# Performance work log

Hardware: AMD Instinct MI355X
Metric: run time of the kernel (lower is better)

The kernel has to match this reference:

```python
import jax, jax.numpy as jnp
import numpy as np

N_NODES = 100000
N_EDGES = 3200000


def setup_inputs() -> dict:
    key = jax.random.key(0)
    ks = jax.random.split(key, 12)
    x = jax.random.normal(ks[0], (N_NODES, 5), dtype=jnp.float32)
    edges = jax.random.randint(ks[1], (2, N_EDGES), 0, N_NODES)
    edge_attr = jax.random.normal(ks[2], (N_EDGES, 2), dtype=jnp.float32)
    detector_labels = jax.random.bernoulli(ks[3], 0.7, (N_NODES,))

    def init(k, shape, fan_in):
        return (jax.random.normal(k, shape, dtype=jnp.float32) / np.sqrt(fan_in)).astype(jnp.float32)

    W_gat = init(ks[4], (5, 16), 5)        # GATConv lin (shared src/dst)
    att_src = init(ks[5], (16,), 16)
    att_dst = init(ks[6], (16,), 16)
    W_edge = init(ks[7], (2, 16), 2)       # GATConv lin_edge
    att_edge = init(ks[8], (16,), 16)
    b_gat = jnp.zeros((16,), jnp.float32)
    W1 = init(ks[9], (34, 64), 34)
    b1 = jnp.zeros((64,), jnp.float32)
    W2 = init(ks[10], (64, 2), 64)
    b2 = jnp.zeros((2,), jnp.float32)
    return dict(x=x, edges=edges, edge_attr=edge_attr, detector_labels=detector_labels,
                W_gat=W_gat, att_src=att_src, att_dst=att_dst, W_edge=W_edge,
                att_edge=att_edge, b_gat=b_gat, W1=W1, b1=b1, W2=W2, b2=b2)


def reference(x, edges, edge_attr, detector_labels, W_gat, att_src, att_dst,
              W_edge, att_edge, b_gat, W1, b1, W2, b2):
    n_nodes = x.shape[0]
    src, dst = edges[0], edges[1]

    # --- GATConv(5 -> 16, heads=1, concat=False, edge_dim=2, no self loops) ---
    h = x @ W_gat                                        # [N, 16]
    a_src = h @ att_src                                  # [N]
    a_dst = h @ att_dst                                  # [N]
    a_edge = (edge_attr @ W_edge) @ att_edge             # [E]
    alpha = jax.nn.leaky_relu(a_src[src] + a_dst[dst] + a_edge, 0.2)
    # segmented softmax over incoming edges of each dst node
    seg_max = jax.ops.segment_max(alpha, dst, num_segments=n_nodes)
    ex = jnp.exp(alpha - seg_max[dst])
    denom = jax.ops.segment_sum(ex, dst, num_segments=n_nodes)
    a = ex / (denom[dst] + 1e-16)                        # [E]
    out = jax.ops.segment_sum(h[src] * a[:, None], dst, num_segments=n_nodes) + b_gat
    xh = jax.nn.relu(out)                                # [N, 16]

    # --- edge update: gather-concat-MLP ---
    feat = jnp.concatenate([xh[src], edge_attr, xh[dst]], axis=-1)   # [E, 34]
    ef = jax.nn.relu(feat @ W1 + b1) @ W2 + b2                       # [E, 2]

    # --- SplitSyndromes: keep edges whose both endpoints are detectors ---
    valid = detector_labels[src] & detector_labels[dst]
    idx = jnp.nonzero(valid)[0]        # eager (data-dependent size, not jitted)
    return edges[:, idx], jax.nn.sigmoid(ef[idx])
```

## Files before the change

kernel.cpp:

```cpp
#include <hip/hip_runtime.h>

#define NN 100000
#define NE 3200000
#define CH 8192
#define NCB ((NE + CH - 1) / CH)
#define ITER (CH / 256)
#define NBK ((NN + 63) >> 6)
#define CAP 2560

typedef __attribute__((ext_vector_type(8))) __bf16 bf16x8;
typedef __attribute__((ext_vector_type(4))) float f32x4;

union BF8 { unsigned short u[8]; bf16x8 v; };

__global__ void kdetect(const unsigned char* __restrict__ lab8, int* __restrict__ flags) {
  __shared__ int tmp[256];
  int t = threadIdx.x;
  int s = 0;
  for (int i = t; i < 25000; i += 256) s += lab8[4 * i + 1];
  tmp[t] = s;
  __syncthreads();
  for (int d = 128; d > 0; d >>= 1) { if (t < d) tmp[t] += tmp[t + d]; __syncthreads(); }
  if (t == 0) flags[0] = (tmp[0] != 0) ? 1 : 0;
}

__global__ void klab(const void* __restrict__ lab, const int* __restrict__ flags,
                     int* __restrict__ labN) {
  int n = blockIdx.x * 256 + threadIdx.x;
  if (n >= NN) return;
  int v;
  if (flags[0]) v = ((const unsigned char*)lab)[n];
  else          v = ((const int*)lab)[n];
  labN[n] = (v != 0) ? 1 : 0;
}

__global__ void kc01(const float* __restrict__ We, const float* __restrict__ ae,
                     float* __restrict__ c01) {
  if (threadIdx.x == 0) {
    float c0 = 0.f, c1 = 0.f;
    for (int k = 0; k < 16; k++) { c0 += We[k] * ae[k]; c1 += We[16 + k] * ae[k]; }
    c01[0] = c0; c01[1] = c1;
  }
}

__global__ void knodeA(const float* __restrict__ x, const float* __restrict__ Wg,
                       const float* __restrict__ atts, const float* __restrict__ attd,
                       float* __restrict__ a_src, float* __restrict__ a_dst) {
  int n = blockIdx.x * 256 + threadIdx.x;
  if (n >= NN) return;
  float xi[5];
#pragma unroll
  for (int i = 0; i < 5; i++) xi[i] = x[n * 5 + i];
  float asum = 0.f, dsum = 0.f;
#pragma unroll
  for (int k = 0; k < 16; k++) {
    float acc = 0.f;
#pragma unroll
    for (int i = 0; i < 5; i++) acc += xi[i] * Wg[i * 16 + k];
    asum += acc * atts[k];
    dsum += acc * attd[k];
  }
  a_src[n] = asum; a_dst[n] = dsum;
}

__global__ __launch_bounds__(256) void khist(const int* __restrict__ src,
                                             const int* __restrict__ dst,
                                             const int* __restrict__ labN,
                                             int* __restrict__ blkcnt,
                                             int* __restrict__ cntc) {
  __shared__ int hist[NBK];
  __shared__ int vsum;
  int tid = threadIdx.x, b = blockIdx.x;
  for (int i = tid; i < NBK; i += 256) hist[i] = 0;
  if (tid == 0) vsum = 0;
  __syncthreads();
  int wsum = 0;
  for (int it = 0; it < ITER; ++it) {
    int e = b * CH + it * 256 + tid;
    int v = 0;
    if (e < NE) {
      int s = src[e], d = dst[e];
      atomicAdd(&hist[d >> 6], 1);
      v = labN[s] & labN[d];
    }
    unsigned long long m = __ballot(v != 0);
    wsum += __popcll(m);
  }
  if ((tid & 63) == 0) atomicAdd(&vsum, wsum);
  __syncthreads();
  for (int i = tid; i < NBK; i += 256) blkcnt[i * NCB + b] = hist[i];
  if (tid == 0) cntc[b] = vsum;
}

__global__ __launch_bounds__(256) void kscanb(int* __restrict__ blkcnt,
                                              int* __restrict__ total) {
  __shared__ int a[512];
  int row = blockIdx.x, t = threadIdx.x;
  int* p = blkcnt + row * NCB;
  int o0 = (t < NCB) ? p[t] : 0;
  int o1 = (t + 256 < NCB) ? p[t + 256] : 0;
  a[t] = o0; a[t + 256] = o1;
  __syncthreads();
  for (int d = 1; d < 512; d <<= 1) {
    int x0 = (t >= d) ? a[t - d] : 0;
    int x1 = (t + 256 >= d) ? a[t + 256 - d] : 0;
    __syncthreads();
    a[t] += x0; a[t + 256] += x1;
    __syncthreads();
  }
  if (t < NCB) p[t] = a[t] - o0;
  if (t + 256 < NCB) p[t + 256] = a[t + 256] - o1;
  if (t == 0) total[row] = a[NCB - 1];
}

__global__ void kscan(const int* __restrict__ cnt, int* __restrict__ off, int nb) {
  __shared__ int tmp[256];
  __shared__ int carry;
  int t = threadIdx.x;
  if (t == 0) carry = 0;
  __syncthreads();
  for (int base = 0; base < nb; base += 256) {
    int i = base + t;
    int v = (i < nb) ? cnt[i] : 0;
    tmp[t] = v;
    __syncthreads();
    for (int d = 1; d < 256; d <<= 1) {
      int add = (t >= d) ? tmp[t - d] : 0;
      __syncthreads();
      tmp[t] += add;
      __syncthreads();
    }
    if (i < nb) off[i] = carry + tmp[t] - v;
    __syncthreads();
    if (t == 0) carry += tmp[255];
    __syncthreads();
  }
  if (t == 0) off[nb] = carry;
}

__global__ __launch_bounds__(256) void kscat(
    const int* __restrict__ src, const int* __restrict__ dst,
    const float* __restrict__ eattr, const int* __restrict__ labN,
    const float* __restrict__ a_src, const float* __restrict__ a_dst,
    const float* __restrict__ c01, const int* __restrict__ bucket_base,
    const int* __restrict__ blkcnt, const int* __restrict__ offc,
    uint2* __restrict__ bins, float* __restrict__ out,
    float2* __restrict__ eat2, int NV) {
  __shared__ int cur[NBK];
  __shared__ int wc[4];
  __shared__ int lbase;
  int b = blockIdx.x, tid = threadIdx.x;
  for (int i = tid; i < NBK; i += 256) cur[i] = bucket_base[i] + blkcnt[i * NCB + b];
  if (tid == 0) lbase = offc[b];
  float c0 = c01[0], c1 = c01[1];
  __syncthreads();
  int lane = tid & 63, wid = tid >> 6;
  for (int it = 0; it < ITER; ++it) {
    int e = b * CH + it * 256 + tid;
    int v = 0, s = 0, d = 0;
    float2 ea;
    if (e < NE) {
      s = src[e]; d = dst[e];
      ea = ((const float2*)eattr)[e];
      float al = a_src[s] + a_dst[d] + ea.x * c0 + ea.y * c1;
      al = (al > 0.f) ? al : 0.2f * al;
      float exv = __expf(al);
      int pos = atomicAdd(&cur[d >> 6], 1);
      uint2 pl;
      pl.x = ((unsigned)s << 6) | (unsigned)(d & 63);
      pl.y = __float_as_uint(exv);
      bins[pos] = pl;
      v = labN[s] & labN[d];
    }
    unsigned long long m = __ballot(v != 0);
    if (lane == 0) wc[wid] = __popcll(m);
    __syncthreads();
    int pre = 0;
    for (int i = 0; i < wid; i++) pre += wc[i];
    pre += __popcll(m & ((1ull << lane) - 1ull));
    if (v) {
      int p = lbase + pre;
      if (p < NV) {
        out[p] = (float)s;
        out[NV + p] = (float)d;
        eat2[p] = ea;
      }
    }
    __syncthreads();
    if (tid == 0) lbase += wc[0] + wc[1] + wc[2] + wc[3];
  }
}

__global__ __launch_bounds__(512) void kagg(
    const uint2* __restrict__ bins, const int* __restrict__ bucket_base,
    const float* __restrict__ x, const float* __restrict__ Wg,
    const float* __restrict__ bg, float* __restrict__ xh) {
  __shared__ uint2 pay[CAP];
  __shared__ int cnt[64], inc[64], cur[64];
  __shared__ float sWg[80], sbg[16];
  int k = blockIdx.x, tid = threadIdx.x;
  if (tid < 80) sWg[tid] = Wg[tid];
  else if (tid < 96) sbg[tid - 80] = bg[tid - 80];
  int start = bucket_base[k], end = bucket_base[k + 1];
  int node0 = k << 6;
  int c = tid & 15, g = tid >> 4;
  __syncthreads();
  float w0 = sWg[c], w1 = sWg[16 + c], w2 = sWg[32 + c], w3 = sWg[48 + c], w4 = sWg[64 + c];
  float acc[2] = {0.f, 0.f}, den[2] = {0.f, 0.f};
  for (int cb = start; cb < end; cb += CAP) {
    int n = min(end - cb, CAP);
    if (tid < 64) cnt[tid] = 0;
    __syncthreads();
    uint2 st0, st1, st2, st3, st4;
    {
      int i;
      i = tid;          if (i < n) { st0 = bins[cb + i]; atomicAdd(&cnt[st0.x & 63], 1); }
      i = tid + 512;    if (i < n) { st1 = bins[cb + i]; atomicAdd(&cnt[st1.x & 63], 1); }
      i = tid + 1024;   if (i < n) { st2 = bins[cb + i]; atomicAdd(&cnt[st2.x & 63], 1); }
      i = tid + 1536;   if (i < n) { st3 = bins[cb + i]; atomicAdd(&cnt[st3.x & 63], 1); }
      i = tid + 2048;   if (i < n) { st4 = bins[cb + i]; atomicAdd(&cnt[st4.x & 63], 1); }
    }
    __syncthreads();
    if (tid < 64) inc[tid] = cnt[tid];
    __syncthreads();
    for (int d = 1; d < 64; d <<= 1) {
      int v = 0;
      if (tid >= d && tid < 64) v = inc[tid - d];
      __syncthreads();
      if (tid < 64) inc[tid] += v;
      __syncthreads();
    }
    if (tid < 64) cur[tid] = inc[tid] - cnt[tid];
    __syncthreads();
    {
      int i;
      i = tid;          if (i < n) pay[atomicAdd(&cur[st0.x & 63], 1)] = st0;
      i = tid + 512;    if (i < n) pay[atomicAdd(&cur[st1.x & 63], 1)] = st1;
      i = tid + 1024;   if (i < n) pay[atomicAdd(&cur[st2.x & 63], 1)] = st2;
      i = tid + 1536;   if (i < n) pay[atomicAdd(&cur[st3.x & 63], 1)] = st3;
      i = tid + 2048;   if (i < n) pay[atomicAdd(&cur[st4.x & 63], 1)] = st4;
    }
    __syncthreads();
#pragma unroll
    for (int p = 0; p < 2; ++p) {
      int nd = p * 32 + g;
      int re = inc[nd], rs = re - cnt[nd];
      float a = 0.f, ds = 0.f;
      for (int idx = rs; idx < re; ++idx) {
        uint2 pl = pay[idx];
        int s = (int)(pl.x >> 6);
        float exv = __uint_as_float(pl.y);
        const float* xp = x + s * 5;
        float h = xp[0] * w0 + xp[1] * w1 + xp[2] * w2 + xp[3] * w3 + xp[4] * w4;
        a += h * exv;
        ds += exv;
      }
      acc[p] += a; den[p] += ds;
    }
    __syncthreads();
  }
#pragma unroll
  for (int p = 0; p < 2; ++p) {
    int node = node0 + p * 32 + g;
    if (node < NN) {
      float dn = fmaxf(den[p], 1e-30f);
      float v = acc[p] / dn + sbg[c];
      xh[node * 16 + c] = (v > 0.f) ? v : 0.f;
    }
  }
}

__global__ __launch_bounds__(256) void kmlp(
    const float2* __restrict__ eat2, const float* __restrict__ xh,
    const float* __restrict__ W1, const float* __restrict__ b1,
    const float* __restrict__ W2, const float* __restrict__ b2,
    float* __restrict__ out, int NV) {
  int tid = threadIdx.x;
  int lane = tid & 63, wid = tid >> 6;
  int lo4 = lane & 15, q = lane >> 4;

  BF8 bh[4], bl[4];
#pragma unroll
  for (int ct = 0; ct < 4; ct++) {
    int col = ct * 16 + lo4;
#pragma unroll
    for (int i = 0; i < 8; i++) {
      int k = q * 8 + i;
      int r = (k < 16) ? k : (k + 2);
      float w = W1[r * 64 + col];
      unsigned u = __float_as_uint(w);
      float rem = w - __uint_as_float(u & 0xffff0000u);
      bh[ct].u[i] = (unsigned short)(u >> 16);
      bl[ct].u[i] = (unsigned short)(__float_as_uint(rem) >> 16);
    }
  }
  float b1v[4], w16v[4], w17v[4], w2a[4], w2b[4];
#pragma unroll
  for (int ct = 0; ct < 4; ct++) {
    int j = ct * 16 + lo4;
    b1v[ct] = b1[j];
    w16v[ct] = W1[16 * 64 + j];
    w17v[ct] = W1[17 * 64 + j];
    w2a[ct] = W2[j * 2 + 0];
    w2b[ct] = W2[j * 2 + 1];
  }
  float bias20 = b2[0], bias21 = b2[1];

  int nwaves = gridDim.x * 4;
  int ntiles = (NV + 15) >> 4;
  for (int tb = blockIdx.x * 4 + wid; tb < ntiles; tb += nwaves) {
    int base = tb * 16;
    BF8 ah, al;
    {
      int p = base + lo4;
      float vals[8] = {0.f, 0.f, 0.f, 0.f, 0.f, 0.f, 0.f, 0.f};
      if (p < NV) {
        int node = (int)out[((q < 2) ? 0 : NV) + p];
        const float4* xp = (const float4*)(xh + node * 16 + (q & 1) * 8);
        float4 f0 = xp[0], f1 = xp[1];
        vals[0] = f0.x; vals[1] = f0.y; vals[2] = f0.z; vals[3] = f0.w;
        vals[4] = f1.x; vals[5] = f1.y; vals[6] = f1.z; vals[7] = f1.w;
      }
#pragma unroll
      for (int i = 0; i < 8; i++) {
        unsigned u = __float_as_uint(vals[i]);
        float rem = vals[i] - __uint_as_float(u & 0xffff0000u);
        ah.u[i] = (unsigned short)(u >> 16);
        al.u[i] = (unsigned short)(__float_as_uint(rem) >> 16);
      }
    }
    f32x4 acc[4];
#pragma unroll
    for (int ct = 0; ct < 4; ct++) {
      f32x4 z = {0.f, 0.f, 0.f, 0.f};
      z = __builtin_amdgcn_mfma_f32_16x16x32_bf16(ah.v, bh[ct].v, z, 0, 0, 0);
      z = __builtin_amdgcn_mfma_f32_16x16x32_bf16(ah.v, bl[ct].v, z, 0, 0, 0);
      z = __builtin_amdgcn_mfma_f32_16x16x32_bf16(al.v, bh[ct].v, z, 0, 0, 0);
      acc[ct] = z;
    }
    float o0[4], o1[4];
#pragma unroll
    for (int reg = 0; reg < 4; reg++) {
      int pr = base + q * 4 + reg;
      float2 ea = make_float2(0.f, 0.f);
      if (pr < NV) ea = eat2[pr];
      float s0 = 0.f, s1 = 0.f;
#pragma unroll
      for (int ct = 0; ct < 4; ct++) {
        float h = acc[ct][reg] + b1v[ct] + ea.x * w16v[ct] + ea.y * w17v[ct];
        h = fmaxf(h, 0.f);
        s0 += h * w2a[ct];
        s1 += h * w2b[ct];
      }
      o0[reg] = s0; o1[reg] = s1;
    }
#pragma unroll
    for (int m = 1; m < 16; m <<= 1) {
#pragma unroll
      for (int reg = 0; reg < 4; reg++) {
        o0[reg] += __shfl_xor(o0[reg], m, 64);
        o1[reg] += __shfl_xor(o1[reg], m, 64);
      }
    }
    if (lo4 == 0) {
#pragma unroll
      for (int reg = 0; reg < 4; reg++) {
        int pr = base + q * 4 + reg;
        if (pr < NV) {
          float v0 = bias20 + o0[reg], v1 = bias21 + o1[reg];
          ((float2*)(out + 2 * (size_t)NV))[pr] = make_float2(
              1.f / (1.f + __expf(-v0)), 1.f / (1.f + __expf(-v1)));
        }
      }
    }
  }
}

static inline size_t al64(size_t v) { return (v + 63) & ~(size_t)63; }

extern "C" void kernel_launch(void* const* d_in, const int* in_sizes, int n_in,
                              void* d_out, int out_size, void* d_ws, size_t ws_size,
                              hipStream_t stream) {
  const float* x     = (const float*)d_in[0];
  const int*   edges = (const int*)d_in[1];
  const float* eattr = (const float*)d_in[2];
  const void*  labels= d_in[3];
  const float* Wg    = (const float*)d_in[4];
  const float* atts  = (const float*)d_in[5];
  const float* attd  = (const float*)d_in[6];
  const float* We    = (const float*)d_in[7];
  const float* atte  = (const float*)d_in[8];
  const float* bg    = (const float*)d_in[9];
  const float* W1    = (const float*)d_in[10];
  const float* b1    = (const float*)d_in[11];
  const float* W2    = (const float*)d_in[12];
  const float* b2    = (const float*)d_in[13];
  float* out = (float*)d_out;
  const int NV = out_size / 4;
  const int* src = edges;
  const int* dst = edges + NE;

  char* w = (char*)d_ws;
  float* xh    = (float*)w;   w += al64((size_t)NN * 64);
  uint2* bins  = (uint2*)w;   w += al64((size_t)NE * 8);
  float2* eat2 = (float2*)w;  w += al64((size_t)NV * 8);
  float* a_src = (float*)w;   w += al64((size_t)NN * 4);
  float* a_dst = (float*)w;   w += al64((size_t)NN * 4);
  int* labN    = (int*)w;     w += al64((size_t)NN * 4);
  int* blkcnt  = (int*)w;     w += al64((size_t)NBK * NCB * 4);
  int* total   = (int*)w;     w += al64((size_t)NBK * 4);
  int* bb      = (int*)w;     w += al64((size_t)(NBK + 1) * 4);
  int* cntc    = (int*)w;     w += al64((size_t)NCB * 4);
  int* offc    = (int*)w;     w += al64((size_t)(NCB + 1) * 4);
  float* c01   = (float*)w;   w += 64;
  int* flags   = (int*)w;     w += 64;

  kdetect<<<1, 256, 0, stream>>>((const unsigned char*)labels, flags);
  klab<<<(NN + 255) / 256, 256, 0, stream>>>(labels, flags, labN);
  kc01<<<1, 64, 0, stream>>>(We, atte, c01);
  knodeA<<<(NN + 255) / 256, 256, 0, stream>>>(x, Wg, atts, attd, a_src, a_dst);
  khist<<<NCB, 256, 0, stream>>>(src, dst, labN, blkcnt, cntc);
  kscanb<<<NBK, 256, 0, stream>>>(blkcnt, total);
  kscan<<<1, 256, 0, stream>>>(total, bb, NBK);
  kscan<<<1, 256, 0, stream>>>(cntc, offc, NCB);
  kscat<<<NCB, 256, 0, stream>>>(src, dst, eattr, labN, a_src, a_dst, c01, bb, blkcnt,
                                 offc, bins, out, eat2, NV);
  kagg<<<NBK, 512, 0, stream>>>(bins, bb, x, Wg, bg, xh);
  if (NV > 0)
    kmlp<<<2048, 256, 0, stream>>>(eat2, xh, W1, b1, W2, b2, out, NV);
}
```

Baseline: 286.3 us.

## Replace per-block bucket count matrix with global atomic bucket cursors

```diff
diff --git a/kernel.cpp b/kernel.cpp
--- a/kernel.cpp
+++ b/kernel.cpp
@@ -7,6 +7,7 @@
 #define ITER (CH / 256)
 #define NBK ((NN + 63) >> 6)
 #define CAP 2560
+#define NWG (NE / 64)
 
 typedef __attribute__((ext_vector_type(8))) __bf16 bf16x8;
 typedef __attribute__((ext_vector_type(4))) float f32x4;
@@ -25,8 +26,9 @@
 }
 
 __global__ void klab(const void* __restrict__ lab, const int* __restrict__ flags,
-                     int* __restrict__ labN) {
+                     int* __restrict__ labN, int* __restrict__ ghist) {
   int n = blockIdx.x * 256 + threadIdx.x;
+  if (n < NBK) ghist[n] = 0;
   if (n >= NN) return;
   int v;
   if (flags[0]) v = ((const unsigned char*)lab)[n];
@@ -66,7 +68,8 @@
 __global__ __launch_bounds__(256) void khist(const int* __restrict__ src,
                                              const int* __restrict__ dst,
                                              const int* __restrict__ labN,
-                                             int* __restrict__ blkcnt,
+                                             int* __restrict__ ghist,
+                                             int* __restrict__ cntw,
                                              int* __restrict__ cntc) {
   __shared__ int hist[NBK];
   __shared__ int vsum;
@@ -74,6 +77,7 @@
   for (int i = tid; i < NBK; i += 256) hist[i] = 0;
   if (tid == 0) vsum = 0;
   __syncthreads();
+  int lane = tid & 63, wid = tid >> 6;
   int wsum = 0;
   for (int it = 0; it < ITER; ++it) {
     int e = b * CH + it * 256 + tid;
@@ -84,33 +88,20 @@
       v = labN[s] & labN[d];
     }
     unsigned long long m = __ballot(v != 0);
-    wsum += __popcll(m);
-  }
-  if ((tid & 63) == 0) atomicAdd(&vsum, wsum);
-  __syncthreads();
-  for (int i = tid; i < NBK; i += 256) blkcnt[i * NCB + b] = hist[i];
+    int c = __popcll(m);
+    if (lane == 0) {
+      int wg = b * 128 + it * 4 + wid;
+      if (wg < NWG) cntw[wg] = c;
+      wsum += c;
+    }
+  }
+  if (lane == 0) atomicAdd(&vsum, wsum);
+  __syncthreads();
+  for (int i = tid; i < NBK; i += 256) {
+    int h = hist[i];
+    if (h) atomicAdd(&ghist[i], h);
+  }
   if (tid == 0) cntc[b] = vsum;
-}
-
-__global__ __launch_bounds__(256) void kscanb(int* __restrict__ blkcnt,
-                                              int* __restrict__ total) {
-  __shared__ int a[512];
-  int row = blockIdx.x, t = threadIdx.x;
-  int* p = blkcnt + row * NCB;
-  int o0 = (t < NCB) ? p[t] : 0;
-  int o1 = (t + 256 < NCB) ? p[t + 256] : 0;
-  a[t] = o0; a[t + 256] = o1;
-  __syncthreads();
-  for (int d = 1; d < 512; d <<= 1) {
-    int x0 = (t >= d) ? a[t - d] : 0;
-    int x1 = (t + 256 >= d) ? a[t + 256 - d] : 0;
-    __syncthreads();
-    a[t] += x0; a[t + 256] += x1;
-    __syncthreads();
-  }
-  if (t < NCB) p[t] = a[t] - o0;
-  if (t + 256 < NCB) p[t + 256] = a[t + 256] - o1;
-  if (t == 0) total[row] = a[NCB - 1];
 }
 
 __global__ void kscan(const int* __restrict__ cnt, int* __restrict__ off, int nb) {
@@ -138,56 +129,66 @@
   if (t == 0) off[nb] = carry;
 }
 
+__global__ __launch_bounds__(256) void kscanw(const int* __restrict__ cntw,
+                                              const int* __restrict__ offc,
+                                              const int* __restrict__ bb,
+                                              int* __restrict__ offw,
+                                              int* __restrict__ gcur) {
+  int b = blockIdx.x, t = threadIdx.x;
+  if (b == 0) {
+    for (int i = t; i < NBK; i += 256) gcur[i * 16] = bb[i];
+  }
+  __shared__ int a[128];
+  int wg = b * 128 + t;
+  int val = 0;
+  if (t < 128) {
+    val = (wg < NWG) ? cntw[wg] : 0;
+    a[t] = val;
+  }
+  __syncthreads();
+  for (int d = 1; d < 128; d <<= 1) {
+    int x = 0;
+    if (t < 128 && t >= d) x = a[t - d];
+    __syncthreads();
+    if (t < 128) a[t] += x;
+    __syncthreads();
+  }
+  if (t < 128 && wg < NWG) offw[wg] = offc[b] + a[t] - val;
+}
+
 __global__ __launch_bounds__(256) void kscat(
     const int* __restrict__ src, const int* __restrict__ dst,
     const float* __restrict__ eattr, const int* __restrict__ labN,
     const float* __restrict__ a_src, const float* __restrict__ a_dst,
-    const float* __restrict__ c01, const int* __restrict__ bucket_base,
-    const int* __restrict__ blkcnt, const int* __restrict__ offc,
-    uint2* __restrict__ bins, float* __restrict__ out,
+    const float* __restrict__ c01, const int* __restrict__ offw,
+    int* __restrict__ gcur, uint2* __restrict__ bins, float* __restrict__ out,
     float2* __restrict__ eat2, int NV) {
-  __shared__ int cur[NBK];
-  __shared__ int wc[4];
-  __shared__ int lbase;
-  int b = blockIdx.x, tid = threadIdx.x;
-  for (int i = tid; i < NBK; i += 256) cur[i] = bucket_base[i] + blkcnt[i * NCB + b];
-  if (tid == 0) lbase = offc[b];
   float c0 = c01[0], c1 = c01[1];
-  __syncthreads();
-  int lane = tid & 63, wid = tid >> 6;
-  for (int it = 0; it < ITER; ++it) {
-    int e = b * CH + it * 256 + tid;
-    int v = 0, s = 0, d = 0;
-    float2 ea;
-    if (e < NE) {
-      s = src[e]; d = dst[e];
-      ea = ((const float2*)eattr)[e];
-      float al = a_src[s] + a_dst[d] + ea.x * c0 + ea.y * c1;
-      al = (al > 0.f) ? al : 0.2f * al;
-      float exv = __expf(al);
-      int pos = atomicAdd(&cur[d >> 6], 1);
-      uint2 pl;
-      pl.x = ((unsigned)s << 6) | (unsigned)(d & 63);
-      pl.y = __float_as_uint(exv);
-      bins[pos] = pl;
-      v = labN[s] & labN[d];
-    }
+  int lane = threadIdx.x & 63;
+  int gw = (blockIdx.x * 256 + threadIdx.x) >> 6;
+  int nw = (gridDim.x * 256) >> 6;
+  for (int wg = gw; wg < NWG; wg += nw) {
+    int e = wg * 64 + lane;
+    int s = src[e], d = dst[e];
+    float2 ea = ((const float2*)eattr)[e];
+    float al = a_src[s] + a_dst[d] + ea.x * c0 + ea.y * c1;
+    al = (al > 0.f) ? al : 0.2f * al;
+    float exv = __expf(al);
+    int pos = atomicAdd(&gcur[(d >> 6) * 16], 1);
+    uint2 pl;
+    pl.x = ((unsigned)s << 6) | (unsigned)(d & 63);
+    pl.y = __float_as_uint(exv);
+    bins[pos] = pl;
+    int v = labN[s] & labN[d];
     unsigned long long m = __ballot(v != 0);
-    if (lane == 0) wc[wid] = __popcll(m);
-    __syncthreads();
-    int pre = 0;
-    for (int i = 0; i < wid; i++) pre += wc[i];
-    pre += __popcll(m & ((1ull << lane) - 1ull));
     if (v) {
-      int p = lbase + pre;
+      int p = offw[wg] + __popcll(m & ((1ull << lane) - 1ull));
       if (p < NV) {
         out[p] = (float)s;
         out[NV + p] = (float)d;
         eat2[p] = ea;
       }
     }
-    __syncthreads();
-    if (tid == 0) lbase += wc[0] + wc[1] + wc[2] + wc[3];
   }
 }
 
@@ -407,24 +408,26 @@
   float* a_src = (float*)w;   w += al64((size_t)NN * 4);
   float* a_dst = (float*)w;   w += al64((size_t)NN * 4);
   int* labN    = (int*)w;     w += al64((size_t)NN * 4);
-  int* blkcnt  = (int*)w;     w += al64((size_t)NBK * NCB * 4);
-  int* total   = (int*)w;     w += al64((size_t)NBK * 4);
+  int* ghist   = (int*)w;     w += al64((size_t)NBK * 4);
   int* bb      = (int*)w;     w += al64((size_t)(NBK + 1) * 4);
   int* cntc    = (int*)w;     w += al64((size_t)NCB * 4);
   int* offc    = (int*)w;     w += al64((size_t)(NCB + 1) * 4);
+  int* cntw    = (int*)w;     w += al64((size_t)NWG * 4);
+  int* offw    = (int*)w;     w += al64((size_t)NWG * 4);
+  int* gcur    = (int*)w;     w += al64((size_t)NBK * 16 * 4);
   float* c01   = (float*)w;   w += 64;
   int* flags   = (int*)w;     w += 64;
 
   kdetect<<<1, 256, 0, stream>>>((const unsigned char*)labels, flags);
-  klab<<<(NN + 255) / 256, 256, 0, stream>>>(labels, flags, labN);
+  klab<<<(NN + 255) / 256, 256, 0, stream>>>(labels, flags, labN, ghist);
   kc01<<<1, 64, 0, stream>>>(We, atte, c01);
   knodeA<<<(NN + 255) / 256, 256, 0, stream>>>(x, Wg, atts, attd, a_src, a_dst);
-  khist<<<NCB, 256, 0, stream>>>(src, dst, labN, blkcnt, cntc);
-  kscanb<<<NBK, 256, 0, stream>>>(blkcnt, total);
-  kscan<<<1, 256, 0, stream>>>(total, bb, NBK);
+  khist<<<NCB, 256, 0, stream>>>(src, dst, labN, ghist, cntw, cntc);
+  kscan<<<1, 256, 0, stream>>>(ghist, bb, NBK);
   kscan<<<1, 256, 0, stream>>>(cntc, offc, NCB);
-  kscat<<<NCB, 256, 0, stream>>>(src, dst, eattr, labN, a_src, a_dst, c01, bb, blkcnt,
-                                 offc, bins, out, eat2, NV);
+  kscanw<<<NCB, 256, 0, stream>>>(cntw, offc, bb, offw, gcur);
+  kscat<<<2048, 256, 0, stream>>>(src, dst, eattr, labN, a_src, a_dst, c01, offw,
+                                  gcur, bins, out, eat2, NV);
   kagg<<<NBK, 512, 0, stream>>>(bins, bb, x, Wg, bg, xh);
   if (NV > 0)
     kmlp<<<2048, 256, 0, stream>>>(eat2, xh, W1, b1, W2, b2, out, NV);
```

Result: slower. 380.2 us (+32.8%).

## Precompute per-wavefront compaction offsets to remove block barriers in scatter

Applied to the files above, without the earlier changes.

```diff
diff --git a/kernel.cpp b/kernel.cpp
--- a/kernel.cpp
+++ b/kernel.cpp
@@ -5,8 +5,10 @@
 #define CH 8192
 #define NCB ((NE + CH - 1) / CH)
 #define ITER (CH / 256)
+#define ITS (CH / 512)
 #define NBK ((NN + 63) >> 6)
 #define CAP 2560
+#define NWG (NE / 64)
 
 typedef __attribute__((ext_vector_type(8))) __bf16 bf16x8;
 typedef __attribute__((ext_vector_type(4))) float f32x4;
@@ -67,6 +69,7 @@
                                              const int* __restrict__ dst,
                                              const int* __restrict__ labN,
                                              int* __restrict__ blkcnt,
+                                             int* __restrict__ cntw,
                                              int* __restrict__ cntc) {
   __shared__ int hist[NBK];
   __shared__ int vsum;
@@ -74,6 +77,7 @@
   for (int i = tid; i < NBK; i += 256) hist[i] = 0;
   if (tid == 0) vsum = 0;
   __syncthreads();
+  int lane = tid & 63, wid = tid >> 6;
   int wsum = 0;
   for (int it = 0; it < ITER; ++it) {
     int e = b * CH + it * 256 + tid;
@@ -84,9 +88,14 @@
       v = labN[s] & labN[d];
     }
     unsigned long long m = __ballot(v != 0);
-    wsum += __popcll(m);
-  }
-  if ((tid & 63) == 0) atomicAdd(&vsum, wsum);
+    int c = __popcll(m);
+    if (lane == 0) {
+      int wg = b * 128 + it * 4 + wid;
+      if (wg < NWG) cntw[wg] = c;
+      wsum += c;
+    }
+  }
+  if (lane == 0) atomicAdd(&vsum, wsum);
   __syncthreads();
   for (int i = tid; i < NBK; i += 256) blkcnt[i * NCB + b] = hist[i];
   if (tid == 0) cntc[b] = vsum;
@@ -138,56 +147,62 @@
   if (t == 0) off[nb] = carry;
 }
 
-__global__ __launch_bounds__(256) void kscat(
+__global__ __launch_bounds__(128) void kscanw(const int* __restrict__ cntw,
+                                              const int* __restrict__ offc,
+                                              int* __restrict__ offw) {
+  int b = blockIdx.x, t = threadIdx.x;
+  __shared__ int a[128];
+  int wg = b * 128 + t;
+  int val = (wg < NWG) ? cntw[wg] : 0;
+  a[t] = val;
+  __syncthreads();
+  for (int d = 1; d < 128; d <<= 1) {
+    int x = (t >= d) ? a[t - d] : 0;
+    __syncthreads();
+    a[t] += x;
+    __syncthreads();
+  }
+  if (wg < NWG) offw[wg] = offc[b] + a[t] - val;
+}
+
+__global__ __launch_bounds__(512) void kscat(
     const int* __restrict__ src, const int* __restrict__ dst,
     const float* __restrict__ eattr, const int* __restrict__ labN,
     const float* __restrict__ a_src, const float* __restrict__ a_dst,
     const float* __restrict__ c01, const int* __restrict__ bucket_base,
-    const int* __restrict__ blkcnt, const int* __restrict__ offc,
+    const int* __restrict__ blkcnt, const int* __restrict__ offw,
     uint2* __restrict__ bins, float* __restrict__ out,
     float2* __restrict__ eat2, int NV) {
   __shared__ int cur[NBK];
-  __shared__ int wc[4];
-  __shared__ int lbase;
   int b = blockIdx.x, tid = threadIdx.x;
-  for (int i = tid; i < NBK; i += 256) cur[i] = bucket_base[i] + blkcnt[i * NCB + b];
-  if (tid == 0) lbase = offc[b];
+  for (int i = tid; i < NBK; i += 512) cur[i] = bucket_base[i] + blkcnt[i * NCB + b];
   float c0 = c01[0], c1 = c01[1];
   __syncthreads();
   int lane = tid & 63, wid = tid >> 6;
-  for (int it = 0; it < ITER; ++it) {
-    int e = b * CH + it * 256 + tid;
-    int v = 0, s = 0, d = 0;
-    float2 ea;
-    if (e < NE) {
-      s = src[e]; d = dst[e];
-      ea = ((const float2*)eattr)[e];
-      float al = a_src[s] + a_dst[d] + ea.x * c0 + ea.y * c1;
-      al = (al > 0.f) ? al : 0.2f * al;
-      float exv = __expf(al);
-      int pos = atomicAdd(&cur[d >> 6], 1);
-      uint2 pl;
-      pl.x = ((unsigned)s << 6) | (unsigned)(d & 63);
-      pl.y = __float_as_uint(exv);
-      bins[pos] = pl;
-      v = labN[s] & labN[d];
-    }
+  for (int it = 0; it < ITS; ++it) {
+    int e = b * CH + it * 512 + tid;
+    if (e >= NE) break;
+    int s = src[e], d = dst[e];
+    float2 ea = ((const float2*)eattr)[e];
+    float al = a_src[s] + a_dst[d] + ea.x * c0 + ea.y * c1;
+    al = (al > 0.f) ? al : 0.2f * al;
+    float exv = __expf(al);
+    int pos = atomicAdd(&cur[d >> 6], 1);
+    uint2 pl;
+    pl.x = ((unsigned)s << 6) | (unsigned)(d & 63);
+    pl.y = __float_as_uint(exv);
+    bins[pos] = pl;
+    int v = labN[s] & labN[d];
     unsigned long long m = __ballot(v != 0);
-    if (lane == 0) wc[wid] = __popcll(m);
-    __syncthreads();
-    int pre = 0;
-    for (int i = 0; i < wid; i++) pre += wc[i];
-    pre += __popcll(m & ((1ull << lane) - 1ull));
     if (v) {
-      int p = lbase + pre;
+      int wg = b * 128 + it * 8 + wid;
+      int p = offw[wg] + __popcll(m & ((1ull << lane) - 1ull));
       if (p < NV) {
         out[p] = (float)s;
         out[NV + p] = (float)d;
         eat2[p] = ea;
       }
     }
-    __syncthreads();
-    if (tid == 0) lbase += wc[0] + wc[1] + wc[2] + wc[3];
   }
 }
 
@@ -412,6 +427,8 @@
   int* bb      = (int*)w;     w += al64((size_t)(NBK + 1) * 4);
   int* cntc    = (int*)w;     w += al64((size_t)NCB * 4);
   int* offc    = (int*)w;     w += al64((size_t)(NCB + 1) * 4);
+  int* cntw    = (int*)w;     w += al64((size_t)NWG * 4);
+  int* offw    = (int*)w;     w += al64((size_t)NWG * 4);
   float* c01   = (float*)w;   w += 64;
   int* flags   = (int*)w;     w += 64;
 
@@ -419,12 +436,13 @@
   klab<<<(NN + 255) / 256, 256, 0, stream>>>(labels, flags, labN);
   kc01<<<1, 64, 0, stream>>>(We, atte, c01);
   knodeA<<<(NN + 255) / 256, 256, 0, stream>>>(x, Wg, atts, attd, a_src, a_dst);
-  khist<<<NCB, 256, 0, stream>>>(src, dst, labN, blkcnt, cntc);
+  khist<<<NCB, 256, 0, stream>>>(src, dst, labN, blkcnt, cntw, cntc);
   kscanb<<<NBK, 256, 0, stream>>>(blkcnt, total);
   kscan<<<1, 256, 0, stream>>>(total, bb, NBK);
   kscan<<<1, 256, 0, stream>>>(cntc, offc, NCB);
-  kscat<<<NCB, 256, 0, stream>>>(src, dst, eattr, labN, a_src, a_dst, c01, bb, blkcnt,
-                                 offc, bins, out, eat2, NV);
+  kscanw<<<NCB, 128, 0, stream>>>(cntw, offc, offw);
+  kscat<<<NCB, 512, 0, stream>>>(src, dst, eattr, labN, a_src, a_dst, c01, bb,
+                                 blkcnt, offw, bins, out, eat2, NV);
   kagg<<<NBK, 512, 0, stream>>>(bins, bb, x, Wg, bg, xh);
   if (NV > 0)
     kmlp<<<2048, 256, 0, stream>>>(eat2, xh, W1, b1, W2, b2, out, NV);
```

Measured after the change: 297.9 us. +4.1%, slower.
